# Kernel optimization log

Hardware: AMD Instinct MI355X
Metric: run time of the kernel (lower is better)

Reference implementation:

```python
import jax, jax.numpy as jnp
import numpy as np

K = 3  # kernel_size
PAD = 1


def _unfold3x3(x):
    # x: [b, c, h, w] -> patches [b, c, k*k, h, w] matching torch.nn.Unfold
    # ordering (row-major over the kernel window, channel outermost).
    b, c, h, w = x.shape
    xp = jnp.pad(x, ((0, 0), (0, 0), (PAD, PAD), (PAD, PAD)))
    patches = jnp.stack(
        [xp[:, :, i:i + h, j:j + w] for i in range(K) for j in range(K)],
        axis=2,
    )
    return patches  # [b, c, 9, h, w]


def setup_inputs() -> dict:
    key = jax.random.key(0)
    k1, k2, k3, k4 = jax.random.split(key, 4)
    b, c, h, w = 8, 64, 128, 128
    out_ch = 64
    x = jax.random.normal(k1, (b, c, h, w), dtype=jnp.float32)
    guide_ch = jax.random.normal(k2, (b, c, h, w), dtype=jnp.float32)
    guide_sp = jax.random.normal(k3, (b, K * K, h, w), dtype=jnp.float32)
    # kaiming_normal_ fan_out on [out, in, k^2, 1, 1]: fan_out = out * k^2 * 1 * 1?
    # torch fan_out for 5D conv weight = out_channels * receptive_field (k^2*1*1)
    fan_out = out_ch * (K * K)
    std = np.sqrt(2.0 / fan_out)
    weight = jax.random.normal(k4, (out_ch, c, K * K), dtype=jnp.float32) * std
    return {"x": x, "guide_ch": guide_ch, "guide_sp": guide_sp, "weight": weight}


def reference(x, guide_ch, guide_sp, weight):
    # filter: [b, c, k^2, h, w] = 1 + tanh(guide_ch[:, :, None] + guide_sp[:, None])
    filt = 1.0 + jnp.tanh(guide_ch[:, :, None, :, :] + guide_sp[:, None, :, :, :])
    patches = _unfold3x3(x)  # [b, c, 9, h, w]
    # conv3d with weight [out, in, k^2, 1, 1] == per-pixel reduction over (c, k^2)
    out = jnp.einsum('bckhw,ock->bohw', patches * filt, weight)
    return out
```

## Files before the change

### kernel.cpp

```cpp
#include <hip/hip_runtime.h>
#include <hip/hip_bf16.h>

typedef short short8 __attribute__((ext_vector_type(8)));
typedef float floatx4 __attribute__((ext_vector_type(4)));
typedef unsigned uintx4 __attribute__((ext_vector_type(4)));

#define HWSZ 16384
#define WD 128
#define CD 64
#define OD 64
#define XSTR 72
#define OSTR 132
#define L2E2 2.8853900817779268f

__device__ __forceinline__ short f2bf(float f) {
    unsigned u = __builtin_bit_cast(unsigned, f);
    u += 0x7FFFu + ((u >> 16) & 1u);
    return (short)(u >> 16);
}

__device__ __forceinline__ unsigned pack2bf(float a, float b) {
    __hip_bfloat162 h = __float22bfloat162_rn(float2{a, b});
    unsigned u;
    __builtin_memcpy(&u, &h, 4);
    return u;
}

__device__ __forceinline__ float bf2f(short s) {
    return __builtin_bit_cast(float, ((unsigned)(unsigned short)s) << 16);
}

__global__ void prepack_w(const float* __restrict__ wgt, unsigned short* __restrict__ wp) {
    int idx = blockIdx.x * 256 + threadIdx.x;
    if (idx < 9 * 64 * 64) {
        int k = idx >> 12, o = (idx >> 6) & 63, c = idx & 63;
        wp[idx] = (unsigned short)f2bf(2.0f * wgt[o * 576 + c * 9 + k]);
    }
}

__global__ __launch_bounds__(256, 3)
void paka_kernel(const float* __restrict__ x, const float* __restrict__ gc,
                 const float* __restrict__ gs, const float* __restrict__ wgt,
                 const unsigned short* __restrict__ wp, float* __restrict__ out)
{
    __shared__ union {
        struct {
            short xl[130 * XSTR];
            short wl[3][64 * XSTR];
        } s;
        float o[64 * OSTR];
    } lds;

    const int tid  = threadIdx.x;
    const int wave = tid >> 6;
    const int lane = tid & 63;
    const int b = blockIdx.x >> 7;
    const int h = blockIdx.x & 127;

    const float* xb  = x  + (size_t)b * CD * HWSZ;
    const float* gcb = gc + (size_t)b * CD * HWSZ;
    const float* gsb = gs + (size_t)b * 9 * HWSZ;

    const int row = lane & 15;
    const int q   = lane >> 4;
    const int mt0 = wave * 2;

    float eg[2][2][8];
    #pragma unroll
    for (int mt = 0; mt < 2; ++mt) {
        int p = (mt0 + mt) * 16 + row;
        #pragma unroll
        for (int ks = 0; ks < 2; ++ks)
            #pragma unroll
            for (int j = 0; j < 8; ++j) {
                int c = ks * 32 + q * 8 + j;
                eg[mt][ks][j] = __builtin_amdgcn_exp2f(gcb[(size_t)c * HWSZ + h * WD + p] * L2E2);
            }
    }
    float esv[9][2];
    #pragma unroll
    for (int k = 0; k < 9; ++k)
        #pragma unroll
        for (int mt = 0; mt < 2; ++mt) {
            int p = (mt0 + mt) * 16 + row;
            esv[k][mt] = __builtin_amdgcn_exp2f(gsb[k * HWSZ + h * WD + p] * L2E2);
        }

    if (tid < 32)
        *(unsigned*)&lds.s.xl[0 * XSTR + tid * 2] = 0u;
    else if (tid < 64)
        *(unsigned*)&lds.s.xl[129 * XSTR + (tid - 32) * 2] = 0u;

    floatx4 acc[2][4];
    #pragma unroll
    for (int i = 0; i < 2; ++i)
        #pragma unroll
        for (int n = 0; n < 4; ++n)
            acc[i][n] = (floatx4){0.f, 0.f, 0.f, 0.f};

    #pragma unroll
    for (int dh = 0; dh < 3; ++dh) {
        const int hh = h + dh - 1;
        if ((unsigned)hh >= 128u) continue;

        __syncthreads();

        if (wp) {
            #pragma unroll
            for (int it = 0; it < 6; ++it) {
                int idx = it * 256 + tid;
                int dw = idx >> 9, o = (idx >> 3) & 63, cg = idx & 7;
                short8 v = *(const short8*)&wp[(dh * 3 + dw) * 4096 + o * 64 + cg * 8];
                *(short8*)&lds.s.wl[dw][o * XSTR + cg * 8] = v;
            }
        } else {
            #pragma unroll
            for (int it = 0; it < 48; ++it) {
                int idx = it * 256 + tid;
                int dw = idx >> 12, o = (idx >> 6) & 63, c = idx & 63;
                lds.s.wl[dw][o * XSTR + c] = f2bf(2.0f * wgt[o * 576 + c * 9 + dh * 3 + dw]);
            }
        }

        {
            const int g = tid >> 5;
            const float* xg = xb + (size_t)(8 * g) * HWSZ + hh * WD;
            #pragma unroll
            for (int it = 0; it < 4; ++it) {
                int p = it * 32 + (tid & 31);
                uintx4 pv;
                #pragma unroll
                for (int cc = 0; cc < 4; ++cc) {
                    float a  = xg[(size_t)(2 * cc) * HWSZ + p];
                    float b2 = xg[(size_t)(2 * cc + 1) * HWSZ + p];
                    pv[cc] = pack2bf(a, b2);
                }
                *(uintx4*)&lds.s.xl[(p + 1) * XSTR + g * 8] = pv;
            }
        }

        __syncthreads();

        #pragma unroll
        for (int dw = 0; dw < 3; ++dw) {
            const int k = dh * 3 + dw;
            #pragma unroll
            for (int ks = 0; ks < 2; ++ks) {
                short8 af[2];
                #pragma unroll
                for (int mt = 0; mt < 2; ++mt) {
                    int wslot = (mt0 + mt) * 16 + row + dw;
                    short8 raw = *(const short8*)&lds.s.xl[wslot * XSTR + ks * 32 + q * 8];
                    float es = esv[k][mt];
                    #pragma unroll
                    for (int jj = 0; jj < 4; ++jj) {
                        float d0 = fmaf(eg[mt][ks][2 * jj],     es, 1.0f);
                        float d1 = fmaf(eg[mt][ks][2 * jj + 1], es, 1.0f);
                        float r0 = __builtin_amdgcn_rcpf(d0);
                        float r1 = __builtin_amdgcn_rcpf(d1);
                        float x0 = bf2f(raw[2 * jj]);
                        float x1 = bf2f(raw[2 * jj + 1]);
                        float t0 = fmaf(-x0, r0, x0);
                        float t1 = fmaf(-x1, r1, x1);
                        ((unsigned*)&af[mt])[jj] = pack2bf(t0, t1);
                    }
                }
                #pragma unroll
                for (int nt = 0; nt < 4; ++nt) {
                    short8 bv = *(const short8*)&lds.s.wl[dw][(nt * 16 + row) * XSTR + ks * 32 + q * 8];
                    acc[0][nt] = __builtin_amdgcn_mfma_f32_16x16x32_bf16(af[0], bv, acc[0][nt], 0, 0, 0);
                    acc[1][nt] = __builtin_amdgcn_mfma_f32_16x16x32_bf16(af[1], bv, acc[1][nt], 0, 0, 0);
                }
            }
        }
    }

    __syncthreads();

    #pragma unroll
    for (int i = 0; i < 2; ++i) {
        int prow = (mt0 + i) * 16 + q * 4;
        #pragma unroll
        for (int nt = 0; nt < 4; ++nt) {
            int o = nt * 16 + row;
            #pragma unroll
            for (int r = 0; r < 4; ++r)
                lds.o[o * OSTR + prow + r] = acc[i][nt][r];
        }
    }

    __syncthreads();

    float* outb = out + ((size_t)b * OD) * HWSZ + h * WD;
    #pragma unroll
    for (int it = 0; it < 8; ++it) {
        int idx = it * 256 + tid;
        int o = idx >> 5, p4 = (idx & 31) * 4;
        *(floatx4*)&outb[(size_t)o * HWSZ + p4] = *(const floatx4*)&lds.o[o * OSTR + p4];
    }
}

extern "C" void kernel_launch(void* const* d_in, const int* in_sizes, int n_in,
                              void* d_out, int out_size, void* d_ws, size_t ws_size,
                              hipStream_t stream) {
    const float* x   = (const float*)d_in[0];
    const float* gcp = (const float*)d_in[1];
    const float* gsp = (const float*)d_in[2];
    const float* wgt = (const float*)d_in[3];
    float* out = (float*)d_out;

    const bool use_wp = ws_size >= (size_t)(9 * 64 * 64 * sizeof(unsigned short));
    unsigned short* wp = use_wp ? (unsigned short*)d_ws : nullptr;
    if (use_wp)
        prepack_w<<<dim3(144), dim3(256), 0, stream>>>(wgt, wp);
    paka_kernel<<<dim3(1024), dim3(256), 0, stream>>>(x, gcp, gsp, wgt, wp, out);
}
```

Baseline: 139.8 us.

## Read weights directly from global, drop LDS weight staging and output transpose

Removes the per-dh LDS staging of the packed weights, so each wave loads its B fragments straight from the prepacked global buffer (L2/L1 resident). The MFMA operands are swapped so the accumulator layout puts output channels along the register dimension, and results are stored directly to global without the LDS transpose pass and its extra barriers. The kernel now uses far less shared memory, and the launch-bounds occupancy hint rises from 3 to 5 blocks. In exchange, the repeated global weight loads add per-wave load latency, and the output stores become scalar 4-byte writes with 64-byte contiguous runs instead of 16-byte vector stores.

```diff
diff --git a/kernel.cpp b/kernel.cpp
--- a/kernel.cpp
+++ b/kernel.cpp
@@ -10,7 +10,6 @@
 #define CD 64
 #define OD 64
 #define XSTR 72
-#define OSTR 132
 #define L2E2 2.8853900817779268f
 
 __device__ __forceinline__ short f2bf(float f) {
@@ -38,18 +37,12 @@
     }
 }
 
-__global__ __launch_bounds__(256, 3)
+__global__ __launch_bounds__(256, 5)
 void paka_kernel(const float* __restrict__ x, const float* __restrict__ gc,
                  const float* __restrict__ gs, const float* __restrict__ wgt,
                  const unsigned short* __restrict__ wp, float* __restrict__ out)
 {
-    __shared__ union {
-        struct {
-            short xl[130 * XSTR];
-            short wl[3][64 * XSTR];
-        } s;
-        float o[64 * OSTR];
-    } lds;
+    __shared__ short xl[130 * XSTR];
 
     const int tid  = threadIdx.x;
     const int wave = tid >> 6;
@@ -87,9 +80,9 @@
         }
 
     if (tid < 32)
-        *(unsigned*)&lds.s.xl[0 * XSTR + tid * 2] = 0u;
+        *(unsigned*)&xl[0 * XSTR + tid * 2] = 0u;
     else if (tid < 64)
-        *(unsigned*)&lds.s.xl[129 * XSTR + (tid - 32) * 2] = 0u;
+        *(unsigned*)&xl[129 * XSTR + (tid - 32) * 2] = 0u;
 
     floatx4 acc[2][4];
     #pragma unroll
@@ -105,23 +98,6 @@
 
         __syncthreads();
 
-        if (wp) {
-            #pragma unroll
-            for (int it = 0; it < 6; ++it) {
-                int idx = it * 256 + tid;
-                int dw = idx >> 9, o = (idx >> 3) & 63, cg = idx & 7;
-                short8 v = *(const short8*)&wp[(dh * 3 + dw) * 4096 + o * 64 + cg * 8];
-                *(short8*)&lds.s.wl[dw][o * XSTR + cg * 8] = v;
-            }
-        } else {
-            #pragma unroll
-            for (int it = 0; it < 48; ++it) {
-                int idx = it * 256 + tid;
-                int dw = idx >> 12, o = (idx >> 6) & 63, c = idx & 63;
-                lds.s.wl[dw][o * XSTR + c] = f2bf(2.0f * wgt[o * 576 + c * 9 + dh * 3 + dw]);
-            }
-        }
-
         {
             const int g = tid >> 5;
             const float* xg = xb + (size_t)(8 * g) * HWSZ + hh * WD;
@@ -135,7 +111,7 @@
                     float b2 = xg[(size_t)(2 * cc + 1) * HWSZ + p];
                     pv[cc] = pack2bf(a, b2);
                 }
-                *(uintx4*)&lds.s.xl[(p + 1) * XSTR + g * 8] = pv;
+                *(uintx4*)&xl[(p + 1) * XSTR + g * 8] = pv;
             }
         }
 
@@ -144,13 +120,14 @@
         #pragma unroll
         for (int dw = 0; dw < 3; ++dw) {
             const int k = dh * 3 + dw;
+            const unsigned short* wk = wp ? wp + k * 4096 : nullptr;
             #pragma unroll
             for (int ks = 0; ks < 2; ++ks) {
                 short8 af[2];
                 #pragma unroll
                 for (int mt = 0; mt < 2; ++mt) {
                     int wslot = (mt0 + mt) * 16 + row + dw;
-                    short8 raw = *(const short8*)&lds.s.xl[wslot * XSTR + ks * 32 + q * 8];
+                    short8 raw = *(const short8*)&xl[wslot * XSTR + ks * 32 + q * 8];
                     float es = esv[k][mt];
                     #pragma unroll
                     for (int jj = 0; jj < 4; ++jj) {
@@ -167,36 +144,35 @@
                 }
                 #pragma unroll
                 for (int nt = 0; nt < 4; ++nt) {
-                    short8 bv = *(const short8*)&lds.s.wl[dw][(nt * 16 + row) * XSTR + ks * 32 + q * 8];
-                    acc[0][nt] = __builtin_amdgcn_mfma_f32_16x16x32_bf16(af[0], bv, acc[0][nt], 0, 0, 0);
-                    acc[1][nt] = __builtin_amdgcn_mfma_f32_16x16x32_bf16(af[1], bv, acc[1][nt], 0, 0, 0);
+                    short8 bv;
+                    if (wk) {
+                        bv = *(const short8*)&wk[(nt * 16 + row) * 64 + ks * 32 + q * 8];
+                    } else {
+                        #pragma unroll
+                        for (int j = 0; j < 8; ++j) {
+                            int o = nt * 16 + row, c = ks * 32 + q * 8 + j;
+                            bv[j] = f2bf(2.0f * wgt[o * 576 + c * 9 + k]);
+                        }
+                    }
+                    acc[0][nt] = __builtin_amdgcn_mfma_f32_16x16x32_bf16(bv, af[0], acc[0][nt], 0, 0, 0);
+                    acc[1][nt] = __builtin_amdgcn_mfma_f32_16x16x32_bf16(bv, af[1], acc[1][nt], 0, 0, 0);
                 }
             }
         }
     }
 
-    __syncthreads();
-
+    float* outb = out + ((size_t)b * OD) * HWSZ + h * WD;
     #pragma unroll
-    for (int i = 0; i < 2; ++i) {
-        int prow = (mt0 + i) * 16 + q * 4;
+    for (int mt = 0; mt < 2; ++mt) {
+        int p = (mt0 + mt) * 16 + row;
         #pragma unroll
         for (int nt = 0; nt < 4; ++nt) {
-            int o = nt * 16 + row;
             #pragma unroll
-            for (int r = 0; r < 4; ++r)
-                lds.o[o * OSTR + prow + r] = acc[i][nt][r];
+            for (int r = 0; r < 4; ++r) {
+                int o = nt * 16 + q * 4 + r;
+                outb[(size_t)o * HWSZ + p] = acc[mt][nt][r];
+            }
         }
-    }
-
-    __syncthreads();
-
-    float* outb = out + ((size_t)b * OD) * HWSZ + h * WD;
-    #pragma unroll
-    for (int it = 0; it < 8; ++it) {
-        int idx = it * 256 + tid;
-        int o = idx >> 5, p4 = (idx & 31) * 4;
-        *(floatx4*)&outb[(size_t)o * HWSZ + p4] = *(const floatx4*)&lds.o[o * OSTR + p4];
     }
 }
 
```

Measured after the change: 178.0 us. 27.3% more time.
